# Kernel tuning notes

Hardware: AMD Instinct MI355X
Metric: run time of the kernel (lower is better)

Reference implementation:

```python
import jax, jax.numpy as jnp
import numpy as np

B, D, H, O, RH, P = 8192, 784, 2048, 1024, 128, 64
NI = NJ = NK = 4  # input regions / hidden groups / output groups


def _make_groups():
    idx = np.arange(28 * 28).reshape(28, 28)
    input_groups = np.stack([
        idx[:14, :14].ravel(), idx[:14, 14:].ravel(),
        idx[14:, :14].ravel(), idx[14:, 14:].ravel(),
    ]).astype(np.int32)                                   # [4, 196]
    hidden_groups = np.arange(H, dtype=np.int32).reshape(NJ, H // NJ)   # [4, 512]
    output_groups = np.arange(O, dtype=np.int32).reshape(NK, O // NK)   # [4, 256]
    return input_groups, hidden_groups, output_groups


def setup_inputs() -> dict:
    key = jax.random.key(0)
    ks = jax.random.split(key, 9)
    ig, hg, og = _make_groups()
    inp = {
        "x":   jax.random.normal(ks[0], (B, D), jnp.float32),
        "W1":  jax.random.normal(ks[1], (H, D), jnp.float32) / np.sqrt(D),
        "b1":  jax.random.normal(ks[2], (H,), jnp.float32) * 0.01,
        "W2":  jax.random.normal(ks[3], (O, H), jnp.float32) / np.sqrt(H),
        "b2":  jax.random.normal(ks[4], (O,), jnp.float32) * 0.01,
        "Wr1": jax.random.normal(ks[5], (RH, D), jnp.float32) / np.sqrt(D),
        "br1": jax.random.normal(ks[6], (RH,), jnp.float32) * 0.01,
        "Wr2": jax.random.normal(ks[7], (P, RH), jnp.float32) / np.sqrt(RH),
        "br2": jax.random.normal(ks[8], (P,), jnp.float32) * 0.01,
        "input_groups": jnp.asarray(ig),
        "hidden_groups": jnp.asarray(hg),
        "output_groups": jnp.asarray(og),
        "top_k": 8,
    }
    return inp


def reference(x, W1, b1, W2, b2, Wr1, br1, Wr2, br2,
              input_groups, hidden_groups, output_groups, top_k):
    # --- router MLP (eval mode: dropout = identity, no routing noise) ---
    h_r = jax.nn.relu(x @ Wr1.T + br1)
    scores = h_r @ Wr2.T + br2                      # [B, P]
    probs = jax.nn.softmax(scores, axis=-1)         # temperature = 1.0

    # --- top-k pathway selection + renormalization ---
    top_vals, top_idx = jax.lax.top_k(probs, top_k)
    bsz = x.shape[0]
    mask = jnp.zeros_like(probs).at[jnp.arange(bsz)[:, None], top_idx].set(top_vals)
    wts = mask / (mask.sum(axis=-1, keepdims=True) + 1e-8)
    wts4 = wts.reshape(bsz, NI, NJ, NK)             # pathway_idx = i*16 + j*4 + k

    # --- gather pathway sub-blocks ---
    x_reg = x[:, input_groups]                      # [B, I, 196]
    # W1g[i, j] = W1[hidden_groups[j]][:, input_groups[i]] -> [I, J, 512, 196]
    W1g = W1[hidden_groups[None, :, :, None], input_groups[:, None, None, :]]
    b1g = b1[hidden_groups]                         # [J, 512]
    # W2g[j, k] = W2[output_groups[k]][:, hidden_groups[j]] -> [J, K, 256, 512]
    W2g = W2[output_groups[None, :, :, None], hidden_groups[:, None, None, :]]
    b2g = b2[output_groups]                         # [K, 256]

    # --- pathway computation (exact erf GELU, as torch F.gelu default) ---
    hidden = jax.nn.gelu(
        jnp.einsum('bin,ijhn->ijbh', x_reg, W1g) + b1g[None, :, None, :],
        approximate=False)                          # [I, J, B, 512]
    # weighted pathway outputs, contracted over i, j, h without materializing
    # the full [I, J, K, B, 256] tensor
    out_main = jnp.einsum('ijbh,jkoh,bijk->bko', hidden, W2g, wts4)  # [B, K, 256]
    wsum = wts4.sum(axis=(1, 2))                    # [B, K] (bias weighted per pathway)
    out_blocks = out_main + wsum[:, :, None] * b2g[None]

    out = jnp.zeros((bsz, O), x.dtype).at[:, output_groups].add(out_blocks)
    return out
```

## Files before the change

### kernel.cpp

```cpp
#include <hip/hip_runtime.h>
#include <hip/hip_bf16.h>
#include <hip/hip_fp16.h>

#define B_  8192
#define D_  784
#define H_  2048
#define O_  1024
#define RH_ 128
#define P_  64
#define KP  224
#define KR  800

typedef __attribute__((ext_vector_type(8))) short short8;
typedef __attribute__((ext_vector_type(8))) _Float16 h16x8;
typedef __attribute__((ext_vector_type(4))) float f32x4;

__device__ inline float bf2f(unsigned short u) {
  union { unsigned int i; float f; } v; v.i = ((unsigned int)u) << 16; return v.f;
}
__device__ inline unsigned short f2bf(float f) {
  __hip_bfloat16 h = __float2bfloat16(f);
  return *reinterpret_cast<unsigned short*>(&h);
}
__device__ inline unsigned short f2h(float f) {
  __half h = __float2half(f);
  return *reinterpret_cast<unsigned short*>(&h);
}
__device__ inline float h2f(unsigned short u) {
  __half h = *reinterpret_cast<__half*>(&u);
  return __half2float(h);
}
__device__ inline float erf_fast(float x) {
  float ax = fabsf(x);
  float t = 1.0f / (1.0f + 0.3275911f * ax);
  float p = ((((1.061405429f * t - 1.453152027f) * t + 1.421413741f) * t
              - 0.284496736f) * t + 0.254829592f) * t;
  float y = 1.0f - p * __expf(-ax * ax);
  return x < 0.f ? -y : y;
}
__device__ inline float gelu_exact(float v) {
  return 0.5f * v * (1.0f + erf_fast(v * 0.70710678118654752f));
}

__device__ inline void gload_lds16(const void* g, void* l) {
  __builtin_amdgcn_global_load_lds((const __attribute__((address_space(1))) void*)g,
                                   (__attribute__((address_space(3))) void*)l, 16, 0, 0);
}

template <bool F16>
__device__ inline void gemm128_db(const unsigned short* gA0, const unsigned short* gA1,
                                  const unsigned short* gB0, const unsigned short* gB1,
                                  int K, char* lds, f32x4 acc[4][4]) {
  const int t = threadIdx.x;
  const int w = t >> 6, l = t & 63;
  const int wr = (w >> 1) * 64, wc = (w & 1) * 64;
  const int lr = l & 15;
  const int swr = (lr >> 1) & 3;
  const int arow = (wr + lr) * 64 + (((l >> 4) ^ swr) * 16);
  const int brow = 8192 + (wc + lr) * 64 + (((l >> 4) ^ swr) * 16);
  const int tOff = t * 16;
  {
    char* d = lds + tOff;
    gload_lds16(gA0, d);
    gload_lds16(gA1, d + 4096);
    gload_lds16(gB0, d + 8192);
    gload_lds16(gB1, d + 12288);
  }
  __syncthreads();
  int cur = 0;
  for (int kt = 0; kt < K; kt += 32) {
    const int nxt = kt + 32;
    if (nxt < K) {
      char* d = lds + ((cur ^ 1) << 14) + tOff;
      gload_lds16(gA0 + nxt, d);
      gload_lds16(gA1 + nxt, d + 4096);
      gload_lds16(gB0 + nxt, d + 8192);
      gload_lds16(gB1 + nxt, d + 12288);
    }
    __builtin_amdgcn_sched_barrier(0);
    const char* buf = lds + (cur << 14);
    short8 af[4], bfr[4];
#pragma unroll
    for (int f = 0; f < 4; ++f) {
      af[f]  = *(const short8*)(buf + arow + f * 1024);
      bfr[f] = *(const short8*)(buf + brow + f * 1024);
    }
#pragma unroll
    for (int fm = 0; fm < 4; ++fm)
#pragma unroll
      for (int fn = 0; fn < 4; ++fn) {
        if constexpr (F16)
          acc[fm][fn] = __builtin_amdgcn_mfma_f32_16x16x32_f16(
              (h16x8)af[fm], (h16x8)bfr[fn], acc[fm][fn], 0, 0, 0);
        else
          acc[fm][fn] = __builtin_amdgcn_mfma_f32_16x16x32_bf16(af[fm], bfr[fn], acc[fm][fn], 0, 0, 0);
      }
    __syncthreads();
    cur ^= 1;
  }
}

__device__ inline void gemm128_db64(const unsigned short* gA0, const unsigned short* gA1,
                                    const unsigned short* gB0, const unsigned short* gB1,
                                    int K, char* lds, f32x4 acc[4][4]) {
  const int t = threadIdx.x;
  const int w = t >> 6, l = t & 63;
  const int wr = (w >> 1) * 64, wc = (w & 1) * 64;
  const int lr = l & 15;
  const int swr = (lr >> 1) & 3;
  const int arow = (wr + lr) * 64 + (((l >> 4) ^ swr) * 16);
  const int brow = 8192 + (wc + lr) * 64 + (((l >> 4) ^ swr) * 16);
  const int tOff = t * 16;
#define STAGE64(bufbase, ksrc) { \
    char* d = lds + (bufbase) + tOff; \
    gload_lds16(gA0 + (ksrc), d); \
    gload_lds16(gA1 + (ksrc), d + 4096); \
    gload_lds16(gB0 + (ksrc), d + 8192); \
    gload_lds16(gB1 + (ksrc), d + 12288); \
    gload_lds16(gA0 + (ksrc) + 32, d + 16384); \
    gload_lds16(gA1 + (ksrc) + 32, d + 16384 + 4096); \
    gload_lds16(gB0 + (ksrc) + 32, d + 16384 + 8192); \
    gload_lds16(gB1 + (ksrc) + 32, d + 16384 + 12288); \
  }
  STAGE64(0, 0);
  __syncthreads();
  int cur = 0;
  for (int kt = 0; kt < K; kt += 64) {
    if (kt + 64 < K) STAGE64((cur ^ 1) << 15, kt + 64);
    __builtin_amdgcn_sched_barrier(0);
    const char* buf = lds + (cur << 15);
#pragma unroll
    for (int c = 0; c < 2; ++c) {
      const char* ch = buf + c * 16384;
      short8 af[4], bfr[4];
#pragma unroll
      for (int f = 0; f < 4; ++f) {
        af[f]  = *(const short8*)(ch + arow + f * 1024);
        bfr[f] = *(const short8*)(ch + brow + f * 1024);
      }
#pragma unroll
      for (int fm = 0; fm < 4; ++fm)
#pragma unroll
        for (int fn = 0; fn < 4; ++fn)
          acc[fm][fn] = __builtin_amdgcn_mfma_f32_16x16x32_bf16(af[fm], bfr[fn], acc[fm][fn], 0, 0, 0);
    }
    __syncthreads();
    cur ^= 1;
  }
#undef STAGE64
}

__device__ inline void gemm128_bt64(const unsigned short* __restrict__ A,
                                    const unsigned short* __restrict__ Bm,
                                    int K, char* lds, f32x4 acc[4][4]) {
  const int t = threadIdx.x;
  const int s_orig = (t & 3) ^ ((t >> 3) & 3);
  const size_t srcOff = (size_t)(t >> 2) * K + s_orig * 8;
  gemm128_db64(A + srcOff, A + srcOff + (size_t)64 * K,
               Bm + srcOff, Bm + srcOff + (size_t)64 * K, K, lds, acc);
}

__global__ void k_prep(const float* __restrict__ x, const float* __restrict__ W1,
                       const float* __restrict__ W2, const int* __restrict__ ig,
                       const float* __restrict__ Wr1,
                       unsigned short* __restrict__ xreg, unsigned short* __restrict__ w1g,
                       unsigned short* __restrict__ w2b,
                       unsigned short* __restrict__ xsp, unsigned short* __restrict__ wr1sp) {
  const size_t N1 = (size_t)4 * B_ * KP;
  const size_t N2 = (size_t)4 * H_ * KP;
  const size_t N3 = (size_t)O_ * H_;
  const size_t N4 = (size_t)B_ * KR;
  const size_t N5 = (size_t)RH_ * KR;
  const size_t TOT = N1 + N2 + N3 + N4 + N5;
  for (size_t idx = (size_t)blockIdx.x * blockDim.x + threadIdx.x; idx < TOT;
       idx += (size_t)gridDim.x * blockDim.x) {
    if (idx < N1) {
      int n = (int)(idx % KP); size_t r = idx / KP;
      int b = (int)(r % B_); int i = (int)(r / B_);
      float v = (n < 196) ? x[(size_t)b * D_ + ig[i * 196 + n]] : 0.f;
      xreg[idx] = f2bf(v);
    } else if (idx < N1 + N2) {
      size_t q = idx - N1;
      int n = (int)(q % KP); size_t r = q / KP;
      int h = (int)(r % H_); int i = (int)(r / H_);
      float v = (n < 196) ? W1[(size_t)h * D_ + ig[i * 196 + n]] : 0.f;
      w1g[q] = f2bf(v);
    } else if (idx < N1 + N2 + N3) {
      size_t q = idx - N1 - N2;
      w2b[q] = f2bf(W2[q]);
    } else if (idx < N1 + N2 + N3 + N4) {
      size_t q = idx - N1 - N2 - N3;
      int c = (int)(q % KR); int b = (int)(q / KR);
      float v = (c < D_) ? x[(size_t)b * D_ + c] : 0.f;
      unsigned short hi = f2h(v);
      unsigned short lo = f2h(v - h2f(hi));
      xsp[(size_t)b * (2 * KR) + c]      = hi;
      xsp[(size_t)b * (2 * KR) + KR + c] = lo;
    } else {
      size_t q = idx - N1 - N2 - N3 - N4;
      int c = (int)(q % KR); int h = (int)(q / KR);
      float v = (c < D_) ? Wr1[(size_t)h * D_ + c] : 0.f;
      unsigned short hi = f2h(v);
      unsigned short lo = f2h(v - h2f(hi));
      wr1sp[(size_t)h * KR + c]                    = hi;
      wr1sp[(size_t)RH_ * KR + h * KR + c]         = hi;
      wr1sp[(size_t)2 * RH_ * KR + h * KR + c]     = lo;
    }
  }
}

__global__ __launch_bounds__(256) void k_r1m(const unsigned short* __restrict__ xsp,
    const unsigned short* __restrict__ wr1sp, float* __restrict__ hrp) {
  __shared__ __align__(128) char lds[32768];
  const int mt = blockIdx.x, z = blockIdx.y;
  const int t = threadIdx.x;
  const int aoff = (z == 1) ? KR : 0;
  const int s_orig = (t & 3) ^ ((t >> 3) & 3);
  const int scol = s_orig * 8;
  const unsigned short* gA0 = xsp + ((size_t)(mt * 128) + (t >> 2)) * (2 * KR) + aoff + scol;
  const unsigned short* gA1 = gA0 + (size_t)64 * (2 * KR);
  const unsigned short* gB0 = wr1sp + (size_t)z * RH_ * KR + (size_t)(t >> 2) * KR + scol;
  const unsigned short* gB1 = gB0 + (size_t)64 * KR;
  f32x4 acc[4][4];
#pragma unroll
  for (int a = 0; a < 4; ++a)
#pragma unroll
    for (int b = 0; b < 4; ++b) acc[a][b] = (f32x4){0.f, 0.f, 0.f, 0.f};
  gemm128_db<true>(gA0, gA1, gB0, gB1, KR, lds, acc);
  float* hz = hrp + (size_t)z * B_ * RH_;
  const int w = t >> 6, l = t & 63;
  const int rbase = mt * 128 + (w >> 1) * 64 + (l >> 4) * 4;
  const int cb = (w & 1) * 64 + (l & 15);
#pragma unroll
  for (int fn = 0; fn < 4; ++fn) {
    const int h = cb + fn * 16;
#pragma unroll
    for (int fm = 0; fm < 4; ++fm)
#pragma unroll
      for (int r = 0; r < 4; ++r)
        hz[(size_t)(rbase + fm * 16 + r) * RH_ + h] = acc[fm][fn][r];
  }
}

#define R2S 32
__global__ __launch_bounds__(256) void k_r2(const float* __restrict__ hrp,
    const float* __restrict__ br1,
    const float* __restrict__ Wr2, const float* __restrict__ br2,
    float* __restrict__ wts, float* __restrict__ wsum,
    unsigned long long* __restrict__ actmask) {
  __shared__ float Ws[64][130];
  __shared__ float hs[R2S][128];
  const int s0 = blockIdx.x * R2S;
  const int t = threadIdx.x;
  for (int idx = t; idx < 2048; idx += 256) {
    int r = idx >> 5, c = (idx & 31) * 4;
    *(float4*)&Ws[r][c] = *(const float4*)(Wr2 + (size_t)r * RH_ + c);
  }
  for (int idx = t; idx < R2S * 32; idx += 256) {
    int r = idx >> 5, c = (idx & 31) * 4;
    const size_t off = (size_t)(s0 + r) * RH_ + c;
    float4 p0 = *(const float4*)(hrp + off);
    float4 p1 = *(const float4*)(hrp + (size_t)1 * B_ * RH_ + off);
    float4 p2 = *(const float4*)(hrp + (size_t)2 * B_ * RH_ + off);
    float4 bb = *(const float4*)(br1 + c);
    float4 s;
    s.x = fmaxf(p0.x + p1.x + p2.x + bb.x, 0.f);
    s.y = fmaxf(p0.y + p1.y + p2.y + bb.y, 0.f);
    s.z = fmaxf(p0.z + p1.z + p2.z + bb.z, 0.f);
    s.w = fmaxf(p0.w + p1.w + p2.w + bb.w, 0.f);
    *(float4*)&hs[r][c] = s;
  }
  __syncthreads();
  const int w = t >> 6, p = t & 63;
  const float wb2 = br2[p];
  for (int si = 0; si < R2S / 4; ++si) {
    const int sl = w * (R2S / 4) + si;
    float sc = wb2;
#pragma unroll
    for (int kk = 0; kk < 32; ++kk) {
      float4 h4 = *(const float4*)&hs[sl][kk * 4];
      float4 w4 = *(const float4*)&Ws[p][kk * 4];
      sc += h4.x * w4.x + h4.y * w4.y + h4.z * w4.z + h4.w * w4.w;
    }
    float m = sc;
#pragma unroll
    for (int o = 32; o; o >>= 1) m = fmaxf(m, __shfl_xor(m, o));
    float e = __expf(sc - m);
    float Z = e;
#pragma unroll
    for (int o = 32; o; o >>= 1) Z += __shfl_xor(Z, o);
    bool sel = false;
    float ssum = 0.f;
    for (int it = 0; it < 8; ++it) {
      float v = sel ? -1.f : e;
      float vm = v;
#pragma unroll
      for (int o = 32; o; o >>= 1) vm = fmaxf(vm, __shfl_xor(vm, o));
      unsigned long long mask = __ballot(!sel && v == vm);
      int first = __ffsll((long long)mask) - 1;
      if (p == first) sel = true;
      ssum += vm;
    }
    const float dn = 1.0f / (ssum + 1e-8f * Z);
    const float wv = sel ? e * dn : 0.f;
    wts[(size_t)(s0 + sl) * 64 + p] = wv;
    const unsigned long long am = __ballot(sel);
    if (p == 0) actmask[s0 + sl] = am;
    float part = wv;
#pragma unroll
    for (int o = 4; o < 64; o <<= 1) part += __shfl_xor(part, o);
    if (p < 4) wsum[(size_t)(s0 + sl) * 4 + p] = part;
  }
}

__global__ __launch_bounds__(256) void k_compact(const unsigned long long* __restrict__ actmask,
                                                 int* __restrict__ lists,
                                                 int* __restrict__ counts) {
  __shared__ int wcnt[4];
  __shared__ int sbase;
  const int ij = blockIdx.x;
  const int shift = (ij >> 2) * 16 + (ij & 3) * 4;
  const int t = threadIdx.x;
  const int wid = t >> 6, lane = t & 63;
  unsigned long long mk[32];
#pragma unroll
  for (int c = 0; c < 32; ++c) mk[c] = actmask[c * 256 + t];
  if (t == 0) sbase = 0;
  __syncthreads();
  for (int c = 0; c < 32; ++c) {
    const int b = c * 256 + t;
    const bool act = ((mk[c] >> shift) & 0xFULL) != 0ULL;
    const unsigned long long m = __ballot(act);
    if (lane == 0) wcnt[wid] = __popcll(m);
    __syncthreads();
    int off = sbase;
    const int tot = wcnt[0] + wcnt[1] + wcnt[2] + wcnt[3];
    for (int q = 0; q < wid; ++q) off += wcnt[q];
    if (act)
      lists[ij * B_ + off + __popcll(m & ((1ULL << lane) - 1ULL))] = b;
    __syncthreads();
    if (t == 0) sbase += tot;
  }
  __syncthreads();
  if (t == 0) counts[ij] = sbase;
}

__global__ __launch_bounds__(256) void k_l1g(const unsigned short* __restrict__ xreg,
    const unsigned short* __restrict__ w1g, const float* __restrict__ b1,
    const int* __restrict__ lists, const int* __restrict__ counts,
    unsigned short* __restrict__ hid16) {
  const int mt = blockIdx.x, nt = blockIdx.y, iq = blockIdx.z;
  const int ij = iq * 4 + (nt >> 2);
  const int count = counts[ij];
  if (mt * 128 >= count) return;
  __shared__ __align__(128) char lds[32768];
  __shared__ int rows[128];
  const int t = threadIdx.x;
  const int* list = lists + (size_t)ij * B_;
  if (t < 128) {
    int rl = mt * 128 + t;
    rows[t] = list[rl < count ? rl : count - 1];
  }
  __syncthreads();
  const int s_orig = (t & 3) ^ ((t >> 3) & 3);
  const int scol = s_orig * 8;
  const int r0 = rows[t >> 2], r1 = rows[(t >> 2) + 64];
  const unsigned short* gA0 = xreg + ((size_t)iq * B_ + r0) * KP + scol;
  const unsigned short* gA1 = xreg + ((size_t)iq * B_ + r1) * KP + scol;
  const unsigned short* gB0 = w1g + ((size_t)(iq * H_ + nt * 128) + (t >> 2)) * KP + scol;
  const unsigned short* gB1 = gB0 + (size_t)64 * KP;
  f32x4 acc[4][4];
#pragma unroll
  for (int a = 0; a < 4; ++a)
#pragma unroll
    for (int b = 0; b < 4; ++b) acc[a][b] = (f32x4){0.f, 0.f, 0.f, 0.f};
  gemm128_db<false>(gA0, gA1, gB0, gB1, KP, lds, acc);
  const int w = t >> 6, l = t & 63;
  const int rloc0 = (w >> 1) * 64 + (l >> 4) * 4;
  const int cloc = (w & 1) * 64 + (l & 15);
  unsigned short* lt = (unsigned short*)lds;
#pragma unroll
  for (int fn = 0; fn < 4; ++fn) {
    const int col = cloc + fn * 16;
    const float bias = b1[nt * 128 + col];
#pragma unroll
    for (int fm = 0; fm < 4; ++fm)
#pragma unroll
      for (int r = 0; r < 4; ++r) {
        const int row = rloc0 + fm * 16 + r;
        const int gsw = (col >> 3) ^ (row & 7);
        lt[row * 128 + gsw * 8 + (col & 7)] = f2h(acc[fm][fn][r] + bias);
      }
  }
  __syncthreads();
  const int mlim = count - mt * 128;
  const int row = t >> 1, half = t & 1;
  if (row < mlim) {
    unsigned short* dst = hid16 + ((size_t)iq * B_ + rows[row]) * H_ + nt * 128 + half * 64;
#pragma unroll
    for (int q = 0; q < 8; ++q) {
      const int g = (half * 8 + q) ^ (row & 7);
      *(short8*)(dst + q * 8) = *(const short8*)(lt + row * 128 + g * 8);
    }
  }
}

__global__ __launch_bounds__(256) void k_combine(unsigned short* __restrict__ hid,
                                                 const float* __restrict__ wts) {
  const int b = blockIdx.x;
  const int n = threadIdx.x * 8;
  const int j = n >> 9;
  const float* wb = wts + (size_t)b * 64 + j * 4;
  float acc[4][8];
#pragma unroll
  for (int k = 0; k < 4; ++k)
#pragma unroll
    for (int e = 0; e < 8; ++e) acc[k][e] = 0.f;
#pragma unroll
  for (int i = 0; i < 4; ++i) {
    const float4 w4 = *(const float4*)(wb + i * 16);
    if (w4.x != 0.f || w4.y != 0.f || w4.z != 0.f || w4.w != 0.f) {
      short8 raw = *(const short8*)(hid + ((size_t)i * B_ + b) * H_ + n);
#pragma unroll
      for (int e = 0; e < 8; ++e) {
        float g = gelu_exact(h2f((unsigned short)raw[e]));
        acc[0][e] += g * w4.x;
        acc[1][e] += g * w4.y;
        acc[2][e] += g * w4.z;
        acc[3][e] += g * w4.w;
      }
    }
  }
#pragma unroll
  for (int k = 0; k < 4; ++k) {
    short8 outv;
#pragma unroll
    for (int e = 0; e < 8; ++e) outv[e] = (short)f2bf(acc[k][e]);
    *(short8*)(hid + ((size_t)k * B_ + b) * H_ + n) = outv;
  }
}

__global__ __launch_bounds__(256) void k_l2(const unsigned short* __restrict__ G,
    const unsigned short* __restrict__ w2b, const float* __restrict__ b2,
    const float* __restrict__ wsum, float* __restrict__ out) {
  __shared__ __align__(128) char lds[65536];
  const int mt = blockIdx.x, nt = blockIdx.y, k = blockIdx.z;
  const unsigned short* A  = G + ((size_t)k * B_ + mt * 128) * H_;
  const unsigned short* Bm = w2b + ((size_t)(k * 256 + nt * 128)) * H_;
  f32x4 acc[4][4];
#pragma unroll
  for (int a = 0; a < 4; ++a)
#pragma unroll
    for (int b = 0; b < 4; ++b) acc[a][b] = (f32x4){0.f, 0.f, 0.f, 0.f};
  gemm128_bt64(A, Bm, H_, lds, acc);
  const int t = threadIdx.x, w = t >> 6, l = t & 63;
  const int rbase = mt * 128 + (w >> 1) * 64 + (l >> 4) * 4;
  const int cb = nt * 128 + (w & 1) * 64 + (l & 15);
#pragma unroll
  for (int fn = 0; fn < 4; ++fn) {
    const int ncol = k * 256 + cb + fn * 16;
    const float bias = b2[ncol];
#pragma unroll
    for (int fm = 0; fm < 4; ++fm)
#pragma unroll
      for (int r = 0; r < 4; ++r) {
        const int m = rbase + fm * 16 + r;
        out[(size_t)m * O_ + ncol] = acc[fm][fn][r] + wsum[m * 4 + k] * bias;
      }
  }
}

extern "C" void kernel_launch(void* const* d_in, const int* in_sizes, int n_in,
                              void* d_out, int out_size, void* d_ws, size_t ws_size,
                              hipStream_t stream) {
  const float* x   = (const float*)d_in[0];
  const float* W1  = (const float*)d_in[1];
  const float* b1  = (const float*)d_in[2];
  const float* W2  = (const float*)d_in[3];
  const float* b2  = (const float*)d_in[4];
  const float* Wr1 = (const float*)d_in[5];
  const float* br1 = (const float*)d_in[6];
  const float* Wr2 = (const float*)d_in[7];
  const float* br2 = (const float*)d_in[8];
  const int*   ig  = (const int*)d_in[9];
  float* out = (float*)d_out;
  char* ws = (char*)d_ws;
  unsigned short* xreg = (unsigned short*)(ws);
  unsigned short* w1g  = (unsigned short*)(ws + 14680064);
  unsigned short* w2b  = (unsigned short*)(ws + 18350080);
  float*          wts  = (float*)(ws + 22544384);
  float*          wsum = (float*)(ws + 24641536);
  unsigned short* hid  = (unsigned short*)(ws + 24772608);
  float*          hrp   = (float*)(ws + 24772608);
  unsigned short* xsp   = (unsigned short*)(ws + 24772608 + 12582912);
  unsigned short* wr1sp = (unsigned short*)(ws + 24772608 + 38797312);
  int*                lists   = (int*)d_out;
  int*                counts  = lists + 16 * B_;
  unsigned long long* actmask = (unsigned long long*)((char*)d_out + 524352);

  k_prep<<<dim3(2048), dim3(256), 0, stream>>>(x, W1, W2, ig, Wr1, xreg, w1g, w2b, xsp, wr1sp);
  k_r1m<<<dim3(B_ / 128, 3), dim3(256), 0, stream>>>(xsp, wr1sp, hrp);
  k_r2<<<dim3(B_ / R2S), dim3(256), 0, stream>>>(hrp, br1, Wr2, br2, wts, wsum, actmask);
  k_compact<<<dim3(16), dim3(256), 0, stream>>>(actmask, lists, counts);
  k_l1g<<<dim3(B_ / 128, H_ / 128, 4), dim3(256), 0, stream>>>(xreg, w1g, b1, lists, counts, hid);
  k_combine<<<dim3(B_), dim3(256), 0, stream>>>(hid, wts);
  k_l2<<<dim3(B_ / 128, 2, 4), dim3(256), 0, stream>>>(hid, w2b, b2, wsum, out);
}
```

Before: 209.4 us.

## Gather routed input rows into compacted contiguous buffer before layer-1 GEMM

Stops k_prep from converting the full dense per-region x tensor and adds a k_prep_m kernel that gathers only the rows each (i,j) pathway routes, into a compacted contiguous bf16 buffer ordered by the routing lists. The layer-1 GEMM then reads A contiguously through the standard tiled loader instead of doing per-row indirect gathers. Rows used by several pathways are now duplicated in the buffer, which needs a larger workspace and one more kernel launch. Prefix offsets are recomputed from counts in each block, and an added barrier protects LDS reuse in the epilogue.

```diff
diff --git a/kernel.cpp b/kernel.cpp
--- a/kernel.cpp
+++ b/kernel.cpp
@@ -98,6 +98,17 @@
     __syncthreads();
     cur ^= 1;
   }
+}
+
+template <bool F16>
+__device__ inline void gemm128_bt(const unsigned short* __restrict__ A,
+                                  const unsigned short* __restrict__ Bm,
+                                  int K, char* lds, f32x4 acc[4][4]) {
+  const int t = threadIdx.x;
+  const int s_orig = (t & 3) ^ ((t >> 3) & 3);
+  const size_t srcOff = (size_t)(t >> 2) * K + s_orig * 8;
+  gemm128_db<F16>(A + srcOff, A + srcOff + (size_t)64 * K,
+                  Bm + srcOff, Bm + srcOff + (size_t)64 * K, K, lds, acc);
 }
 
 __device__ inline void gemm128_db64(const unsigned short* gA0, const unsigned short* gA1,
@@ -160,36 +171,28 @@
                Bm + srcOff, Bm + srcOff + (size_t)64 * K, K, lds, acc);
 }
 
-__global__ void k_prep(const float* __restrict__ x, const float* __restrict__ W1,
-                       const float* __restrict__ W2, const int* __restrict__ ig,
-                       const float* __restrict__ Wr1,
-                       unsigned short* __restrict__ xreg, unsigned short* __restrict__ w1g,
-                       unsigned short* __restrict__ w2b,
-                       unsigned short* __restrict__ xsp, unsigned short* __restrict__ wr1sp) {
-  const size_t N1 = (size_t)4 * B_ * KP;
+__global__ void k_prep_r(const float* __restrict__ x, const float* __restrict__ W1,
+                         const float* __restrict__ W2, const int* __restrict__ ig,
+                         const float* __restrict__ Wr1,
+                         unsigned short* __restrict__ w1g, unsigned short* __restrict__ w2b,
+                         unsigned short* __restrict__ xsp, unsigned short* __restrict__ wr1sp) {
   const size_t N2 = (size_t)4 * H_ * KP;
   const size_t N3 = (size_t)O_ * H_;
   const size_t N4 = (size_t)B_ * KR;
   const size_t N5 = (size_t)RH_ * KR;
-  const size_t TOT = N1 + N2 + N3 + N4 + N5;
+  const size_t TOT = N2 + N3 + N4 + N5;
   for (size_t idx = (size_t)blockIdx.x * blockDim.x + threadIdx.x; idx < TOT;
        idx += (size_t)gridDim.x * blockDim.x) {
-    if (idx < N1) {
+    if (idx < N2) {
       int n = (int)(idx % KP); size_t r = idx / KP;
-      int b = (int)(r % B_); int i = (int)(r / B_);
-      float v = (n < 196) ? x[(size_t)b * D_ + ig[i * 196 + n]] : 0.f;
-      xreg[idx] = f2bf(v);
-    } else if (idx < N1 + N2) {
-      size_t q = idx - N1;
-      int n = (int)(q % KP); size_t r = q / KP;
       int h = (int)(r % H_); int i = (int)(r / H_);
       float v = (n < 196) ? W1[(size_t)h * D_ + ig[i * 196 + n]] : 0.f;
-      w1g[q] = f2bf(v);
-    } else if (idx < N1 + N2 + N3) {
-      size_t q = idx - N1 - N2;
+      w1g[idx] = f2bf(v);
+    } else if (idx < N2 + N3) {
+      size_t q = idx - N2;
       w2b[q] = f2bf(W2[q]);
-    } else if (idx < N1 + N2 + N3 + N4) {
-      size_t q = idx - N1 - N2 - N3;
+    } else if (idx < N2 + N3 + N4) {
+      size_t q = idx - N2 - N3;
       int c = (int)(q % KR); int b = (int)(q / KR);
       float v = (c < D_) ? x[(size_t)b * D_ + c] : 0.f;
       unsigned short hi = f2h(v);
@@ -197,7 +200,7 @@
       xsp[(size_t)b * (2 * KR) + c]      = hi;
       xsp[(size_t)b * (2 * KR) + KR + c] = lo;
     } else {
-      size_t q = idx - N1 - N2 - N3 - N4;
+      size_t q = idx - N2 - N3 - N4;
       int c = (int)(q % KR); int h = (int)(q / KR);
       float v = (c < D_) ? Wr1[(size_t)h * D_ + c] : 0.f;
       unsigned short hi = f2h(v);
@@ -345,7 +348,34 @@
   if (t == 0) counts[ij] = sbase;
 }
 
-__global__ __launch_bounds__(256) void k_l1g(const unsigned short* __restrict__ xreg,
+__global__ __launch_bounds__(256) void k_prep_m(const float* __restrict__ x,
+    const int* __restrict__ ig, const int* __restrict__ lists,
+    const int* __restrict__ counts, unsigned short* __restrict__ xregc) {
+  const int ij = blockIdx.y;
+  const int i = ij >> 2;
+  const int cnt = counts[ij];
+  const int s0 = blockIdx.x * 128;
+  if (s0 >= cnt) return;
+  int off = 0;
+  for (int q = 0; q < 16; ++q) if (q < ij) off += counts[q];
+  const int t = threadIdx.x;
+  const int* cm = ig + i * 196;
+  for (int c = t; c < 128 * 28; c += 256) {
+    const int sl = s0 + c / 28;
+    if (sl >= cnt) break;
+    const int nc = (c % 28) * 8;
+    const float* xr = x + (size_t)lists[ij * B_ + sl] * D_;
+    short8 v;
+#pragma unroll
+    for (int e = 0; e < 8; ++e) {
+      const int n = nc + e;
+      v[e] = (short)f2bf(n < 196 ? xr[cm[n]] : 0.f);
+    }
+    *(short8*)(xregc + (size_t)(off + sl) * KP + nc) = v;
+  }
+}
+
+__global__ __launch_bounds__(256) void k_l1g(const unsigned short* __restrict__ xregc,
     const unsigned short* __restrict__ w1g, const float* __restrict__ b1,
     const int* __restrict__ lists, const int* __restrict__ counts,
     unsigned short* __restrict__ hid16) {
@@ -356,29 +386,27 @@
   __shared__ __align__(128) char lds[32768];
   __shared__ int rows[128];
   const int t = threadIdx.x;
+  int off = 0;
+  for (int q = 0; q < 16; ++q) if (q < ij) off += counts[q];
   const int* list = lists + (size_t)ij * B_;
   if (t < 128) {
     int rl = mt * 128 + t;
     rows[t] = list[rl < count ? rl : count - 1];
   }
   __syncthreads();
-  const int s_orig = (t & 3) ^ ((t >> 3) & 3);
-  const int scol = s_orig * 8;
-  const int r0 = rows[t >> 2], r1 = rows[(t >> 2) + 64];
-  const unsigned short* gA0 = xreg + ((size_t)iq * B_ + r0) * KP + scol;
-  const unsigned short* gA1 = xreg + ((size_t)iq * B_ + r1) * KP + scol;
-  const unsigned short* gB0 = w1g + ((size_t)(iq * H_ + nt * 128) + (t >> 2)) * KP + scol;
-  const unsigned short* gB1 = gB0 + (size_t)64 * KP;
+  const unsigned short* A  = xregc + (size_t)(off + mt * 128) * KP;
+  const unsigned short* Bm = w1g + (size_t)(iq * H_ + nt * 128) * KP;
   f32x4 acc[4][4];
 #pragma unroll
   for (int a = 0; a < 4; ++a)
 #pragma unroll
     for (int b = 0; b < 4; ++b) acc[a][b] = (f32x4){0.f, 0.f, 0.f, 0.f};
-  gemm128_db<false>(gA0, gA1, gB0, gB1, KP, lds, acc);
+  gemm128_bt<false>(A, Bm, KP, lds, acc);
   const int w = t >> 6, l = t & 63;
   const int rloc0 = (w >> 1) * 64 + (l >> 4) * 4;
   const int cloc = (w & 1) * 64 + (l & 15);
   unsigned short* lt = (unsigned short*)lds;
+  __syncthreads();
 #pragma unroll
   for (int fn = 0; fn < 4; ++fn) {
     const int col = cloc + fn * 16;
@@ -485,24 +513,25 @@
   const int*   ig  = (const int*)d_in[9];
   float* out = (float*)d_out;
   char* ws = (char*)d_ws;
-  unsigned short* xreg = (unsigned short*)(ws);
-  unsigned short* w1g  = (unsigned short*)(ws + 14680064);
-  unsigned short* w2b  = (unsigned short*)(ws + 18350080);
-  float*          wts  = (float*)(ws + 22544384);
-  float*          wsum = (float*)(ws + 24641536);
-  unsigned short* hid  = (unsigned short*)(ws + 24772608);
-  float*          hrp   = (float*)(ws + 24772608);
-  unsigned short* xsp   = (unsigned short*)(ws + 24772608 + 12582912);
-  unsigned short* wr1sp = (unsigned short*)(ws + 24772608 + 38797312);
+  unsigned short* xregc = (unsigned short*)(ws);
+  unsigned short* w1g   = (unsigned short*)(ws + 29491200);
+  unsigned short* w2b   = (unsigned short*)(ws + 33161216);
+  float*          wts   = (float*)(ws + 37355520);
+  float*          wsum  = (float*)(ws + 39452672);
+  unsigned short* hid   = (unsigned short*)(ws + 39583744);
+  float*          hrp   = (float*)(ws + 39583744);
+  unsigned short* xsp   = (unsigned short*)(ws + 39583744 + 12582912);
+  unsigned short* wr1sp = (unsigned short*)(ws + 39583744 + 38797312);
   int*                lists   = (int*)d_out;
   int*                counts  = lists + 16 * B_;
   unsigned long long* actmask = (unsigned long long*)((char*)d_out + 524352);
 
-  k_prep<<<dim3(2048), dim3(256), 0, stream>>>(x, W1, W2, ig, Wr1, xreg, w1g, w2b, xsp, wr1sp);
+  k_prep_r<<<dim3(2048), dim3(256), 0, stream>>>(x, W1, W2, ig, Wr1, w1g, w2b, xsp, wr1sp);
   k_r1m<<<dim3(B_ / 128, 3), dim3(256), 0, stream>>>(xsp, wr1sp, hrp);
   k_r2<<<dim3(B_ / R2S), dim3(256), 0, stream>>>(hrp, br1, Wr2, br2, wts, wsum, actmask);
   k_compact<<<dim3(16), dim3(256), 0, stream>>>(actmask, lists, counts);
-  k_l1g<<<dim3(B_ / 128, H_ / 128, 4), dim3(256), 0, stream>>>(xreg, w1g, b1, lists, counts, hid);
+  k_prep_m<<<dim3(64, 16), dim3(256), 0, stream>>>(x, ig, lists, counts, xregc);
+  k_l1g<<<dim3(B_ / 128, H_ / 128, 4), dim3(256), 0, stream>>>(xregc, w1g, b1, lists, counts, hid);
   k_combine<<<dim3(B_), dim3(256), 0, stream>>>(hid, wts);
   k_l2<<<dim3(B_ / 128, 2, 4), dim3(256), 0, stream>>>(hid, w2b, b2, wsum, out);
 }
```

Result: slower. 277.6 us (+32.5%).
